# Kernel tuning notes

Measured on AMD Instinct MI355X. Metric: run time of the kernel, lower is better.

Reference implementation:

```python
import jax, jax.numpy as jnp
import numpy as np

HEADS = 16
DIM_HEAD = 64
SCALE = DIM_HEAD ** -0.5

def setup_inputs() -> dict:
    key = jax.random.key(0)
    k1, k2, k3 = jax.random.split(key, 3)
    dim = HEADS * DIM_HEAD  # 1024
    x = jax.random.normal(k1, (2, 4096, dim), dtype=jnp.float32)
    w_qkv = jax.random.normal(k2, (dim, 3 * dim), dtype=jnp.float32) * (dim ** -0.5)
    w_out = jax.random.normal(k3, (dim, dim), dtype=jnp.float32) * (dim ** -0.5)
    return {"x": x, "w_qkv": w_qkv, "w_out": w_out}

def reference(x, w_qkv, w_out):
    b, n, dim = x.shape
    qkv = x @ w_qkv  # (b, n, 3*h*d)
    qkv = qkv.reshape(b, n, 3, HEADS, DIM_HEAD)
    q, k, v = (qkv[:, :, 0], qkv[:, :, 1], qkv[:, :, 2])  # (b, n, h, d)
    q = jnp.swapaxes(q, 1, 2) * SCALE  # (b, h, n, d)
    k = jnp.swapaxes(k, 1, 2)
    v = jnp.swapaxes(v, 1, 2)
    sim = jnp.einsum('bhid,bhjd->bhij', q, k)
    mask_value = -jnp.finfo(sim.dtype).max
    causal_mask = jnp.triu(jnp.ones((n, n), dtype=bool), k=1)
    sim = jnp.where(causal_mask, mask_value, sim)
    attn = jax.nn.softmax(sim, axis=-1)
    out = jnp.einsum('bhij,bhjd->bhid', attn, v)
    out = jnp.swapaxes(out, 1, 2).reshape(b, n, HEADS * DIM_HEAD)
    return out @ w_out
```

## Files before the change

kernel.cpp:

```cpp
#include <hip/hip_runtime.h>
#include <stdint.h>
#include <stddef.h>

typedef __attribute__((ext_vector_type(8))) short bf16x8;
typedef __attribute__((ext_vector_type(4))) float f32x4;
typedef __attribute__((ext_vector_type(4))) unsigned short u16x4;
typedef __attribute__((ext_vector_type(4))) unsigned int u32x4;

#define BATCH 2
#define SEQ 4096
#define NHEADS 16
#define DHEAD 64
#define DIM 1024
#define MTOT 8192
#define N1 3072
#define NEGINF -3.0e4f

__device__ __forceinline__ unsigned short f2bf(float f) {
  union { float f; unsigned u; } x; x.f = f;
  unsigned r = x.u + 0x7fffu + ((x.u >> 16) & 1u);
  return (unsigned short)(r >> 16);
}

__device__ __forceinline__ unsigned pk_bf16(float a, float b) {
  unsigned d;
  asm("v_cvt_pk_bf16_f32 %0, %1, %2" : "=v"(d) : "v"(a), "v"(b));
  return d;
}

__device__ __forceinline__ void gload_lds16(const void* g, void* l) {
  __builtin_amdgcn_global_load_lds(
      (const __attribute__((address_space(1))) void*)g,
      (__attribute__((address_space(3))) void*)l, 16, 0, 0);
}

__global__ __launch_bounds__(256) void cvt_f2b(const float* __restrict__ in,
                                               unsigned short* __restrict__ out,
                                               int n4) {
  int i = blockIdx.x * 256 + threadIdx.x;
  if (i < n4) {
    f32x4 v = ((const f32x4*)in)[i];
    u16x4 o;
#pragma unroll
    for (int j = 0; j < 4; j++) o[j] = f2bf(v[j]);
    ((u16x4*)out)[i] = o;
  }
}

__global__ void transpose_cvt(const float* __restrict__ in,
                              unsigned short* __restrict__ out, int R, int C) {
  __shared__ unsigned short t[32][33];
  int tx = threadIdx.x, ty = threadIdx.y;
  int c0 = blockIdx.x * 32, r0 = blockIdx.y * 32;
#pragma unroll
  for (int i = 0; i < 4; i++)
    t[ty + i * 8][tx] = f2bf(in[(size_t)(r0 + ty + i * 8) * C + c0 + tx]);
  __syncthreads();
#pragma unroll
  for (int i = 0; i < 4; i++)
    out[(size_t)(c0 + ty + i * 8) * R + r0 + tx] = t[tx][ty + i * 8];
}

template <int MODE>
__global__ __launch_bounds__(256) void gemm_bt(
    const unsigned short* __restrict__ A,
    const unsigned short* __restrict__ Bt,
    unsigned short* __restrict__ O0,
    unsigned short* __restrict__ O1,
    unsigned short* __restrict__ O2,
    float* __restrict__ Of,
    int N, int K) {
  __shared__ unsigned short Asl[128][32];
  __shared__ unsigned short Bsl[128][32];
  const int tid = threadIdx.x;
  const int lane = tid & 63, wv = tid >> 6;
  const int wr = wv >> 1, wc = wv & 1;
  const int m0 = blockIdx.x * 128, n0 = blockIdx.y * 128;
  const int lrow = lane >> 2, lcol = (lane & 3) * 8;
  const int fr = lane & 15, kc8 = (lane >> 4) * 8;
  f32x4 acc[4][4] = {};
  for (int k0 = 0; k0 < K; k0 += 32) {
#pragma unroll
    for (int c = 0; c < 2; c++) {
      int r = wv * 32 + c * 16 + lrow;
      gload_lds16(&A[(size_t)(m0 + r) * K + k0 + lcol], &Asl[wv * 32 + c * 16][0]);
      gload_lds16(&Bt[(size_t)(n0 + r) * K + k0 + lcol], &Bsl[wv * 32 + c * 16][0]);
    }
    __syncthreads();
    bf16x8 af[4], bfr[4];
#pragma unroll
    for (int i = 0; i < 4; i++)
      af[i] = *(const bf16x8*)&Asl[wr * 64 + i * 16 + fr][kc8];
#pragma unroll
    for (int j = 0; j < 4; j++)
      bfr[j] = *(const bf16x8*)&Bsl[wc * 64 + j * 16 + fr][kc8];
#pragma unroll
    for (int i = 0; i < 4; i++)
#pragma unroll
      for (int j = 0; j < 4; j++)
        acc[i][j] = __builtin_amdgcn_mfma_f32_16x16x32_bf16(af[i], bfr[j], acc[i][j], 0, 0, 0);
    __syncthreads();
  }
  const int rq = (lane >> 4) * 4;
#pragma unroll
  for (int i = 0; i < 4; i++) {
#pragma unroll
    for (int j = 0; j < 4; j++) {
#pragma unroll
      for (int r = 0; r < 4; r++) {
        int row = m0 + wr * 64 + i * 16 + rq + r;
        int col = n0 + wc * 64 + j * 16 + fr;
        float v = acc[i][j][r];
        if (MODE == 0) {
          int w = col >> 10, rem = col & 1023;
          int h = rem >> 6, d = rem & 63;
          int b = row >> 12, n = row & 4095;
          size_t bh = (size_t)b * NHEADS + h;
          if (w == 0)      O0[(bh * SEQ + n) * DHEAD + d] = f2bf(v * 0.125f);
          else if (w == 1) O1[(bh * SEQ + n) * DHEAD + d] = f2bf(v);
          else             O2[(bh * DHEAD + d) * SEQ + n] = f2bf(v);
        } else {
          Of[(size_t)row * N + col] = v;
        }
      }
    }
  }
}

__device__ __forceinline__ void attn_tile4(
    int tq, const unsigned short* __restrict__ Qp,
    const unsigned short* __restrict__ Kp,
    const unsigned short* __restrict__ Vp,
    unsigned short* __restrict__ AOp,
    unsigned short* __restrict__ Kl,
    unsigned short* __restrict__ Vl,
    int lane, int wv) {
  const int fr = lane & 15, g = lane >> 4;
  const int kc8 = g * 8, rq = g * 4;
  const int sw = fr & 7;
  const int q0 = tq * 128;
  const int srl = lane >> 3;
  const int jl = lane & 7;
  const int ktmax = 2 * tq + 1;

  bf16x8 qf[2][2];
#pragma unroll
  for (int s = 0; s < 2; s++)
#pragma unroll
    for (int c = 0; c < 2; c++)
      qf[s][c] = *(const bf16x8*)&Qp[(size_t)(q0 + wv * 32 + s * 16 + fr) * DHEAD + c * 32 + kc8];

  f32x4 oacc[2][4] = {};
  float mrow[2] = {NEGINF, NEGINF};
  float lrow[2] = {0.f, 0.f};

#pragma unroll
  for (int c = 0; c < 2; c++) {
    int seg = wv * 2 + c;
    int r = seg * 8 + srl;
    int j = jl ^ (r & 7);
    gload_lds16(&Kp[(size_t)r * DHEAD + j * 8], Kl + seg * 512);
    gload_lds16(&Vp[(size_t)r * SEQ + j * 8], Vl + seg * 512);
  }
  __syncthreads();

  int cur = 0;
  for (int kt = 0; kt <= ktmax; kt++) {
    const int ktn = (kt < ktmax) ? kt + 1 : ktmax;
    unsigned short* Kc = Kl + cur * 4096;
    unsigned short* Vc = Vl + cur * 4096;
    unsigned short* Kn = Kl + (cur ^ 1) * 4096;
    unsigned short* Vn = Vl + (cur ^ 1) * 4096;
#pragma unroll
    for (int c = 0; c < 2; c++) {
      int seg = wv * 2 + c;
      int r = seg * 8 + srl;
      int j = jl ^ (r & 7);
      gload_lds16(&Kp[(size_t)(ktn * 64 + r) * DHEAD + j * 8], Kn + seg * 512);
      gload_lds16(&Vp[(size_t)r * SEQ + ktn * 64 + j * 8], Vn + seg * 512);
    }
    f32x4 sv[2][4];
    __builtin_amdgcn_s_setprio(1);
#pragma unroll
    for (int cb = 0; cb < 4; cb++) {
      bf16x8 kf0 = *(const bf16x8*)&Kc[(cb * 16 + fr) * 64 + ((g ^ sw) << 3)];
      bf16x8 kf1 = *(const bf16x8*)&Kc[(cb * 16 + fr) * 64 + (((4 + g) ^ sw) << 3)];
      f32x4 z0 = {};
      z0 = __builtin_amdgcn_mfma_f32_16x16x32_bf16(kf0, qf[0][0], z0, 0, 0, 0);
      sv[0][cb] = __builtin_amdgcn_mfma_f32_16x16x32_bf16(kf1, qf[0][1], z0, 0, 0, 0);
      f32x4 z1 = {};
      z1 = __builtin_amdgcn_mfma_f32_16x16x32_bf16(kf0, qf[1][0], z1, 0, 0, 0);
      sv[1][cb] = __builtin_amdgcn_mfma_f32_16x16x32_bf16(kf1, qf[1][1], z1, 0, 0, 0);
    }
    __builtin_amdgcn_s_setprio(0);
    if (kt >= 2 * tq) {
      const int delta = (kt - 2 * tq) << 6;
#pragma unroll
      for (int s = 0; s < 2; s++)
#pragma unroll
        for (int cb = 0; cb < 4; cb++)
#pragma unroll
          for (int r = 0; r < 4; r++)
            if (cb * 16 + rq + r + delta > wv * 32 + s * 16 + fr)
              sv[s][cb][r] = NEGINF;
    }
    bf16x8 pa[2][2];
#pragma unroll
    for (int s = 0; s < 2; s++) {
      float c0 = fmaxf(fmaxf(sv[s][0][0], sv[s][0][1]), fmaxf(sv[s][0][2], sv[s][0][3]));
      float c1 = fmaxf(fmaxf(sv[s][1][0], sv[s][1][1]), fmaxf(sv[s][1][2], sv[s][1][3]));
      float c2 = fmaxf(fmaxf(sv[s][2][0], sv[s][2][1]), fmaxf(sv[s][2][2], sv[s][2][3]));
      float c3 = fmaxf(fmaxf(sv[s][3][0], sv[s][3][1]), fmaxf(sv[s][3][2], sv[s][3][3]));
      float pmax = fmaxf(fmaxf(c0, c1), fmaxf(c2, c3));
      pmax = fmaxf(pmax, __shfl_xor(pmax, 16, 64));
      pmax = fmaxf(pmax, __shfl_xor(pmax, 32, 64));
      float mnew = fmaxf(mrow[s], pmax);
      float alpha = __expf(mrow[s] - mnew);
      float a0 = __shfl(alpha, rq + 0, 64);
      float a1 = __shfl(alpha, rq + 1, 64);
      float a2 = __shfl(alpha, rq + 2, 64);
      float a3 = __shfl(alpha, rq + 3, 64);
#pragma unroll
      for (int db = 0; db < 4; db++) {
        oacc[s][db][0] *= a0; oacc[s][db][1] *= a1;
        oacc[s][db][2] *= a2; oacc[s][db][3] *= a3;
      }
      lrow[s] *= alpha;
      mrow[s] = mnew;
#pragma unroll
      for (int cb = 0; cb < 4; cb++)
#pragma unroll
        for (int r = 0; r < 4; r++)
          sv[s][cb][r] = __expf(sv[s][cb][r] - mnew);
      float t0 = (sv[s][0][0] + sv[s][0][1]) + (sv[s][0][2] + sv[s][0][3]);
      float t1 = (sv[s][1][0] + sv[s][1][1]) + (sv[s][1][2] + sv[s][1][3]);
      float t2 = (sv[s][2][0] + sv[s][2][1]) + (sv[s][2][2] + sv[s][2][3]);
      float t3 = (sv[s][3][0] + sv[s][3][1]) + (sv[s][3][2] + sv[s][3][3]);
      float lsum = (t0 + t1) + (t2 + t3);
      lsum += __shfl_xor(lsum, 16, 64);
      lsum += __shfl_xor(lsum, 32, 64);
      lrow[s] += lsum;
      unsigned A0 = pk_bf16(sv[s][0][0], sv[s][0][1]), A1 = pk_bf16(sv[s][0][2], sv[s][0][3]);
      unsigned B0 = pk_bf16(sv[s][1][0], sv[s][1][1]), B1 = pk_bf16(sv[s][1][2], sv[s][1][3]);
      unsigned C0 = pk_bf16(sv[s][2][0], sv[s][2][1]), C1 = pk_bf16(sv[s][2][2], sv[s][2][3]);
      unsigned D0 = pk_bf16(sv[s][3][0], sv[s][3][1]), D1 = pk_bf16(sv[s][3][2], sv[s][3][3]);
      const bool lo2 = (g < 2);
      unsigned R0 = __shfl_xor((int)(lo2 ? B0 : A0), 32, 64);
      unsigned R1 = __shfl_xor((int)(lo2 ? B1 : A1), 32, 64);
      unsigned R2 = __shfl_xor((int)(lo2 ? D0 : C0), 32, 64);
      unsigned R3 = __shfl_xor((int)(lo2 ? D1 : C1), 32, 64);
      unsigned o00 = (g == 0) ? A0 : (g == 3) ? B0 : R0;
      unsigned o01 = (g == 0) ? A1 : (g == 3) ? B1 : R1;
      unsigned o10 = (g == 0) ? C0 : (g == 3) ? D0 : R2;
      unsigned o11 = (g == 0) ? C1 : (g == 3) ? D1 : R3;
      unsigned p00 = (g == 1) ? A0 : (g == 2) ? B0 : R0;
      unsigned p01 = (g == 1) ? A1 : (g == 2) ? B1 : R1;
      unsigned p10 = (g == 1) ? C0 : (g == 2) ? D0 : R2;
      unsigned p11 = (g == 1) ? C1 : (g == 2) ? D1 : R3;
      unsigned x00 = __shfl_xor((int)p00, 16, 64);
      unsigned x01 = __shfl_xor((int)p01, 16, 64);
      unsigned x10 = __shfl_xor((int)p10, 16, 64);
      unsigned x11 = __shfl_xor((int)p11, 16, 64);
      const bool odd = (g & 1);
      u32x4 f0, f1;
      f0[0] = odd ? x00 : o00; f0[1] = odd ? x01 : o01;
      f0[2] = odd ? o00 : x00; f0[3] = odd ? o01 : x01;
      f1[0] = odd ? x10 : o10; f1[1] = odd ? x11 : o11;
      f1[2] = odd ? o10 : x10; f1[3] = odd ? o11 : x11;
      pa[s][0] = *(bf16x8*)&f0;
      pa[s][1] = *(bf16x8*)&f1;
    }
    __builtin_amdgcn_s_setprio(1);
#pragma unroll
    for (int db = 0; db < 4; db++) {
      bf16x8 vf0 = *(const bf16x8*)&Vc[(db * 16 + fr) * 64 + ((g ^ sw) << 3)];
      bf16x8 vf1 = *(const bf16x8*)&Vc[(db * 16 + fr) * 64 + (((4 + g) ^ sw) << 3)];
      oacc[0][db] = __builtin_amdgcn_mfma_f32_16x16x32_bf16(pa[0][0], vf0, oacc[0][db], 0, 0, 0);
      oacc[0][db] = __builtin_amdgcn_mfma_f32_16x16x32_bf16(pa[0][1], vf1, oacc[0][db], 0, 0, 0);
      oacc[1][db] = __builtin_amdgcn_mfma_f32_16x16x32_bf16(pa[1][0], vf0, oacc[1][db], 0, 0, 0);
      oacc[1][db] = __builtin_amdgcn_mfma_f32_16x16x32_bf16(pa[1][1], vf1, oacc[1][db], 0, 0, 0);
    }
    __builtin_amdgcn_s_setprio(0);
    __syncthreads();
    cur ^= 1;
  }

#pragma unroll
  for (int s = 0; s < 2; s++) {
    float i0 = __builtin_amdgcn_rcpf(__shfl(lrow[s], rq + 0, 64));
    float i1 = __builtin_amdgcn_rcpf(__shfl(lrow[s], rq + 1, 64));
    float i2 = __builtin_amdgcn_rcpf(__shfl(lrow[s], rq + 2, 64));
    float i3 = __builtin_amdgcn_rcpf(__shfl(lrow[s], rq + 3, 64));
    int nb = q0 + wv * 32 + s * 16 + rq;
#pragma unroll
    for (int db = 0; db < 4; db++) {
      int d = db * 16 + fr;
      AOp[(size_t)(nb + 0) * DIM + d] = f2bf(oacc[s][db][0] * i0);
      AOp[(size_t)(nb + 1) * DIM + d] = f2bf(oacc[s][db][1] * i1);
      AOp[(size_t)(nb + 2) * DIM + d] = f2bf(oacc[s][db][2] * i2);
      AOp[(size_t)(nb + 3) * DIM + d] = f2bf(oacc[s][db][3] * i3);
    }
  }
}

__global__ __launch_bounds__(256, 2) void attn_causal(
    const unsigned short* __restrict__ Q,
    const unsigned short* __restrict__ Kb,
    const unsigned short* __restrict__ Vt,
    unsigned short* __restrict__ AO) {
  const int id = blockIdx.x;
  const int xcd = id & 7, t = id >> 3;
  const int pi = t & 15, bq = t >> 4;
  const int bh = xcd * 4 + bq;
  const int tid = threadIdx.x, lane = tid & 63, wv = tid >> 6;

  const unsigned short* Qp = Q + (size_t)bh * SEQ * DHEAD;
  const unsigned short* Kp = Kb + (size_t)bh * SEQ * DHEAD;
  const unsigned short* Vp = Vt + (size_t)bh * DHEAD * SEQ;
  const int b = bh >> 4, h = bh & 15;
  unsigned short* AOp = AO + (size_t)b * SEQ * DIM + h * DHEAD;

  __shared__ unsigned short Kl[2][4096];
  __shared__ unsigned short Vl[2][4096];

  attn_tile4(pi, Qp, Kp, Vp, AOp, &Kl[0][0], &Vl[0][0], lane, wv);
  attn_tile4(31 - pi, Qp, Kp, Vp, AOp, &Kl[0][0], &Vl[0][0], lane, wv);
}

extern "C" void kernel_launch(void* const* d_in, const int* in_sizes, int n_in,
                              void* d_out, int out_size, void* d_ws, size_t ws_size,
                              hipStream_t stream) {
  const float* x    = (const float*)d_in[0];
  const float* wqkv = (const float*)d_in[1];
  const float* wout = (const float*)d_in[2];
  float* out = (float*)d_out;

  unsigned short* ws = (unsigned short*)d_ws;
  unsigned short* xb = ws;
  unsigned short* ao = ws;
  unsigned short* wqkv_t = ws + (size_t)MTOT * DIM;
  unsigned short* wout_t = wqkv_t + (size_t)N1 * DIM;
  unsigned short* qb = wout_t + (size_t)DIM * DIM;
  unsigned short* kb = qb + (size_t)BATCH * NHEADS * SEQ * DHEAD;
  unsigned short* vt = kb + (size_t)BATCH * NHEADS * SEQ * DHEAD;

  int n4 = (MTOT * DIM) / 4;
  hipLaunchKernelGGL(cvt_f2b, dim3(n4 / 256), dim3(256), 0, stream, x, xb, n4);

  dim3 tb(32, 8);
  hipLaunchKernelGGL(transpose_cvt, dim3(N1 / 32, DIM / 32), tb, 0, stream,
                     wqkv, wqkv_t, DIM, N1);
  hipLaunchKernelGGL(transpose_cvt, dim3(DIM / 32, DIM / 32), tb, 0, stream,
                     wout, wout_t, DIM, DIM);

  hipLaunchKernelGGL((gemm_bt<0>), dim3(MTOT / 128, N1 / 128), dim3(256), 0, stream,
                     xb, wqkv_t, qb, kb, vt, nullptr, N1, DIM);

  hipLaunchKernelGGL(attn_causal, dim3(512), dim3(256), 0, stream,
                     qb, kb, vt, ao);

  hipLaunchKernelGGL((gemm_bt<1>), dim3(MTOT / 128, DIM / 128), dim3(256), 0, stream,
                     ao, wout_t, nullptr, nullptr, nullptr, out, DIM, DIM);
}
```

Measured before the change: 273.9 us.

## Use 256-row query tiles with 8 waves per attention block

The causal attention kernel now gives each block one 256-row query tile handled by 8 waves (512 threads), instead of two 128-row tiles paired for balance and run back to back by 4 waves. Each K/V tile loaded into LDS is shared by twice as many query rows, which halves K/V global traffic per query row. Each wave now loads one K/V segment instead of two. Blocks are ordered so heavy and light causal tiles interleave across XCDs. In exchange, each block's work is more uneven, more blocks may share a CU, and the diagonal tiles carry more masked waste.

```diff
diff --git a/kernel.cpp b/kernel.cpp
--- a/kernel.cpp
+++ b/kernel.cpp
@@ -127,7 +127,7 @@
   }
 }
 
-__device__ __forceinline__ void attn_tile4(
+__device__ __forceinline__ void attn_tile5(
     int tq, const unsigned short* __restrict__ Qp,
     const unsigned short* __restrict__ Kp,
     const unsigned short* __restrict__ Vp,
@@ -138,10 +138,10 @@
   const int fr = lane & 15, g = lane >> 4;
   const int kc8 = g * 8, rq = g * 4;
   const int sw = fr & 7;
-  const int q0 = tq * 128;
+  const int q0 = tq * 256;
   const int srl = lane >> 3;
   const int jl = lane & 7;
-  const int ktmax = 2 * tq + 1;
+  const int ktmax = 4 * tq + 3;
 
   bf16x8 qf[2][2];
 #pragma unroll
@@ -154,13 +154,11 @@
   float mrow[2] = {NEGINF, NEGINF};
   float lrow[2] = {0.f, 0.f};
 
-#pragma unroll
-  for (int c = 0; c < 2; c++) {
-    int seg = wv * 2 + c;
-    int r = seg * 8 + srl;
+  {
+    int r = wv * 8 + srl;
     int j = jl ^ (r & 7);
-    gload_lds16(&Kp[(size_t)r * DHEAD + j * 8], Kl + seg * 512);
-    gload_lds16(&Vp[(size_t)r * SEQ + j * 8], Vl + seg * 512);
+    gload_lds16(&Kp[(size_t)r * DHEAD + j * 8], Kl + wv * 512);
+    gload_lds16(&Vp[(size_t)r * SEQ + j * 8], Vl + wv * 512);
   }
   __syncthreads();
 
@@ -171,13 +169,11 @@
     unsigned short* Vc = Vl + cur * 4096;
     unsigned short* Kn = Kl + (cur ^ 1) * 4096;
     unsigned short* Vn = Vl + (cur ^ 1) * 4096;
-#pragma unroll
-    for (int c = 0; c < 2; c++) {
-      int seg = wv * 2 + c;
-      int r = seg * 8 + srl;
+    {
+      int r = wv * 8 + srl;
       int j = jl ^ (r & 7);
-      gload_lds16(&Kp[(size_t)(ktn * 64 + r) * DHEAD + j * 8], Kn + seg * 512);
-      gload_lds16(&Vp[(size_t)r * SEQ + ktn * 64 + j * 8], Vn + seg * 512);
+      gload_lds16(&Kp[(size_t)(ktn * 64 + r) * DHEAD + j * 8], Kn + wv * 512);
+      gload_lds16(&Vp[(size_t)r * SEQ + ktn * 64 + j * 8], Vn + wv * 512);
     }
     f32x4 sv[2][4];
     __builtin_amdgcn_s_setprio(1);
@@ -193,8 +189,8 @@
       sv[1][cb] = __builtin_amdgcn_mfma_f32_16x16x32_bf16(kf1, qf[1][1], z1, 0, 0, 0);
     }
     __builtin_amdgcn_s_setprio(0);
-    if (kt >= 2 * tq) {
-      const int delta = (kt - 2 * tq) << 6;
+    if (kt >= 4 * tq) {
+      const int delta = (kt - 4 * tq) << 6;
 #pragma unroll
       for (int s = 0; s < 2; s++)
 #pragma unroll
@@ -303,15 +299,18 @@
   }
 }
 
-__global__ __launch_bounds__(256, 2) void attn_causal(
+__global__ __launch_bounds__(512, 4) void attn_causal(
     const unsigned short* __restrict__ Q,
     const unsigned short* __restrict__ Kb,
     const unsigned short* __restrict__ Vt,
     unsigned short* __restrict__ AO) {
   const int id = blockIdx.x;
-  const int xcd = id & 7, t = id >> 3;
-  const int pi = t & 15, bq = t >> 4;
-  const int bh = xcd * 4 + bq;
+  const int xcd = id & 7;
+  const int inner = id >> 3;
+  const int s = inner & 31;
+  const int r = inner >> 5;
+  const int tq = r ? (15 - (s & 15)) : (s & 15);
+  const int bh = xcd * 4 + 2 * r + (s >> 4);
   const int tid = threadIdx.x, lane = tid & 63, wv = tid >> 6;
 
   const unsigned short* Qp = Q + (size_t)bh * SEQ * DHEAD;
@@ -323,8 +322,7 @@
   __shared__ unsigned short Kl[2][4096];
   __shared__ unsigned short Vl[2][4096];
 
-  attn_tile4(pi, Qp, Kp, Vp, AOp, &Kl[0][0], &Vl[0][0], lane, wv);
-  attn_tile4(31 - pi, Qp, Kp, Vp, AOp, &Kl[0][0], &Vl[0][0], lane, wv);
+  attn_tile5(tq, Qp, Kp, Vp, AOp, &Kl[0][0], &Vl[0][0], lane, wv);
 }
 
 extern "C" void kernel_launch(void* const* d_in, const int* in_sizes, int n_in,
@@ -356,7 +354,7 @@
   hipLaunchKernelGGL((gemm_bt<0>), dim3(MTOT / 128, N1 / 128), dim3(256), 0, stream,
                      xb, wqkv_t, qb, kb, vt, nullptr, N1, DIM);
 
-  hipLaunchKernelGGL(attn_causal, dim3(512), dim3(256), 0, stream,
+  hipLaunchKernelGGL(attn_causal, dim3(512), dim3(512), 0, stream,
                      qb, kb, vt, ao);
 
   hipLaunchKernelGGL((gemm_bt<1>), dim3(MTOT / 128, DIM / 128), dim3(256), 0, stream,
```

Measured after the change: 279.0 us. No clear change (+1.8%).
